# Kernel optimization log

Measured on AMD Instinct MI355X. Metric: run time of the kernel, lower is better.

Reference implementation:

```python
import jax, jax.numpy as jnp
import numpy as np

B, D, L = 16384, 1024, 3


def setup_inputs() -> dict:
    key = jax.random.key(0)
    kx, kw, kb = jax.random.split(key, 3)
    # xavier_normal for a (D, 1) tensor: std = sqrt(2 / (D + 1))
    std = float(np.sqrt(2.0 / (D + 1)))
    x = jax.random.normal(kx, (B, D), dtype=jnp.float32)
    weights = jax.random.normal(kw, (L, D), dtype=jnp.float32) * std
    bias = jax.random.normal(kb, (L, D), dtype=jnp.float32) * std
    return {"x": x, "weights": weights, "bias": bias}


def reference(x, weights, bias):
    # DCN cross layer: xl_{t+1} = x0 * (xl_t . w_t) + b_t + xl_t
    # (identical math to matmul(x0 xl^T, w) + b + xl, without the [B,D,D] intermediate)
    x0 = x

    def layer(xl, wb):
        w, b = wb  # [D], [D]
        s = xl @ w  # [B] scaled dot-product reduction
        xl_new = x0 * s[:, None] + b + xl  # [B, D]
        return xl_new, None

    out, _ = jax.lax.scan(layer, x, (weights, bias))
    return out
```

## Files before the change

kernel.cpp:

```cpp
#include <hip/hip_runtime.h>


#define CN_B 16384
#define CN_D 1024
#define CN_L 3
#define ROWS_PER_WAVE 2
#define WAVES_PER_BLOCK 4
#define ROWS_PER_BLOCK (ROWS_PER_WAVE * WAVES_PER_BLOCK)

__global__ __launch_bounds__(256, 4) void crossnet_kernel(
    const float* __restrict__ x,
    const float* __restrict__ w,
    const float* __restrict__ bias,
    float* __restrict__ out) {
  const int tid  = threadIdx.x;
  const int wave = tid >> 6;
  const int lane = tid & 63;
  const int row0 = (blockIdx.x * WAVES_PER_BLOCK + wave) * ROWS_PER_WAVE;

  const float4* xr0 = reinterpret_cast<const float4*>(x + (size_t)row0 * CN_D);
  const float4* xr1 = reinterpret_cast<const float4*>(x + (size_t)(row0 + 1) * CN_D);

  float4 x0a[4], xla[4], x0b[4], xlb[4];
  #pragma unroll
  for (int k = 0; k < 4; ++k) {
    x0a[k] = xr0[k * 64 + lane];
    x0b[k] = xr1[k * 64 + lane];
    xla[k] = x0a[k];
    xlb[k] = x0b[k];
  }

  #pragma unroll
  for (int l = 0; l < CN_L; ++l) {
    const float4* wrow = reinterpret_cast<const float4*>(w    + l * CN_D);
    const float4* brow = reinterpret_cast<const float4*>(bias + l * CN_D);
    float4 wl[4], bl[4];
    #pragma unroll
    for (int k = 0; k < 4; ++k) {
      wl[k] = wrow[k * 64 + lane];
      bl[k] = brow[k * 64 + lane];
    }

    float pa = 0.0f, pb = 0.0f;
    #pragma unroll
    for (int k = 0; k < 4; ++k) {
      pa += xla[k].x * wl[k].x; pb += xlb[k].x * wl[k].x;
      pa += xla[k].y * wl[k].y; pb += xlb[k].y * wl[k].y;
      pa += xla[k].z * wl[k].z; pb += xlb[k].z * wl[k].z;
      pa += xla[k].w * wl[k].w; pb += xlb[k].w * wl[k].w;
    }

    #pragma unroll
    for (int off = 32; off > 0; off >>= 1) {
      pa += __shfl_xor(pa, off, 64);
      pb += __shfl_xor(pb, off, 64);
    }

    #pragma unroll
    for (int k = 0; k < 4; ++k) {
      xla[k].x = x0a[k].x * pa + bl[k].x + xla[k].x;
      xla[k].y = x0a[k].y * pa + bl[k].y + xla[k].y;
      xla[k].z = x0a[k].z * pa + bl[k].z + xla[k].z;
      xla[k].w = x0a[k].w * pa + bl[k].w + xla[k].w;
      xlb[k].x = x0b[k].x * pb + bl[k].x + xlb[k].x;
      xlb[k].y = x0b[k].y * pb + bl[k].y + xlb[k].y;
      xlb[k].z = x0b[k].z * pb + bl[k].z + xlb[k].z;
      xlb[k].w = x0b[k].w * pb + bl[k].w + xlb[k].w;
    }
  }

  float4* or0 = reinterpret_cast<float4*>(out + (size_t)row0 * CN_D);
  float4* or1 = reinterpret_cast<float4*>(out + (size_t)(row0 + 1) * CN_D);
  #pragma unroll
  for (int k = 0; k < 4; ++k) {
    or0[k * 64 + lane] = xla[k];
    or1[k * 64 + lane] = xlb[k];
  }
}

extern "C" void kernel_launch(void* const* d_in, const int* in_sizes, int n_in,
                              void* d_out, int out_size, void* d_ws, size_t ws_size,
                              hipStream_t stream) {
  const float* x    = (const float*)d_in[0];
  const float* w    = (const float*)d_in[1];
  const float* bias = (const float*)d_in[2];
  float* out        = (float*)d_out;

  crossnet_kernel<<<CN_B / ROWS_PER_BLOCK, 256, 0, stream>>>(x, w, bias, out);
}
```

Before: 25.55 us.

## Collapse three cross layers into closed-form scalar recurrence with single batched reduction

Every layer's output has the form x0*alpha + accumulated bias, so the kernel precomputes all three x0·w_l dot products and the bias·weight constants in one pass. It then finishes every wave reduction in one batched shuffle phase instead of three serialized ones. The output is written as x0*alpha plus the summed bias. This removes the dependent reduction chain and the per-layer register updates. In exchange each lane carries more accumulators and loads all weights up front, and the floating-point summation order changes.

```diff
diff --git a/kernel.cpp b/kernel.cpp
--- a/kernel.cpp
+++ b/kernel.cpp
@@ -3,10 +3,13 @@
 
 #define CN_B 16384
 #define CN_D 1024
-#define CN_L 3
 #define ROWS_PER_WAVE 2
 #define WAVES_PER_BLOCK 4
 #define ROWS_PER_BLOCK (ROWS_PER_WAVE * WAVES_PER_BLOCK)
+
+__device__ __forceinline__ float dot4(const float4 a, const float4 b) {
+  return a.x * b.x + a.y * b.y + a.z * b.z + a.w * b.w;
+}
 
 __global__ __launch_bounds__(256, 4) void crossnet_kernel(
     const float* __restrict__ x,
@@ -20,61 +23,78 @@
 
   const float4* xr0 = reinterpret_cast<const float4*>(x + (size_t)row0 * CN_D);
   const float4* xr1 = reinterpret_cast<const float4*>(x + (size_t)(row0 + 1) * CN_D);
+  const float4* w0r = reinterpret_cast<const float4*>(w);
+  const float4* w1r = reinterpret_cast<const float4*>(w + CN_D);
+  const float4* w2r = reinterpret_cast<const float4*>(w + 2 * CN_D);
+  const float4* b0r = reinterpret_cast<const float4*>(bias);
+  const float4* b1r = reinterpret_cast<const float4*>(bias + CN_D);
+  const float4* b2r = reinterpret_cast<const float4*>(bias + 2 * CN_D);
 
-  float4 x0a[4], xla[4], x0b[4], xlb[4];
+  float4 x0a[4], x0b[4];
   #pragma unroll
   for (int k = 0; k < 4; ++k) {
     x0a[k] = xr0[k * 64 + lane];
     x0b[k] = xr1[k * 64 + lane];
-    xla[k] = x0a[k];
-    xlb[k] = x0b[k];
+  }
+
+  float da0 = 0.f, da1 = 0.f, da2 = 0.f;
+  float db0 = 0.f, db1 = 0.f, db2 = 0.f;
+  float c1 = 0.f, c2 = 0.f;
+  float4 bs[4];
+
+  #pragma unroll
+  for (int k = 0; k < 4; ++k) {
+    const int idx = k * 64 + lane;
+    const float4 w0 = w0r[idx];
+    const float4 w1 = w1r[idx];
+    const float4 w2 = w2r[idx];
+    const float4 b0 = b0r[idx];
+    const float4 b1 = b1r[idx];
+    const float4 b2 = b2r[idx];
+
+    da0 += dot4(x0a[k], w0);  db0 += dot4(x0b[k], w0);
+    da1 += dot4(x0a[k], w1);  db1 += dot4(x0b[k], w1);
+    da2 += dot4(x0a[k], w2);  db2 += dot4(x0b[k], w2);
+
+    c1 += dot4(b0, w1);
+    float4 b01;
+    b01.x = b0.x + b1.x; b01.y = b0.y + b1.y;
+    b01.z = b0.z + b1.z; b01.w = b0.w + b1.w;
+    c2 += dot4(b01, w2);
+    bs[k].x = b01.x + b2.x; bs[k].y = b01.y + b2.y;
+    bs[k].z = b01.z + b2.z; bs[k].w = b01.w + b2.w;
   }
 
   #pragma unroll
-  for (int l = 0; l < CN_L; ++l) {
-    const float4* wrow = reinterpret_cast<const float4*>(w    + l * CN_D);
-    const float4* brow = reinterpret_cast<const float4*>(bias + l * CN_D);
-    float4 wl[4], bl[4];
-    #pragma unroll
-    for (int k = 0; k < 4; ++k) {
-      wl[k] = wrow[k * 64 + lane];
-      bl[k] = brow[k * 64 + lane];
-    }
+  for (int off = 32; off > 0; off >>= 1) {
+    da0 += __shfl_xor(da0, off, 64);
+    da1 += __shfl_xor(da1, off, 64);
+    da2 += __shfl_xor(da2, off, 64);
+    db0 += __shfl_xor(db0, off, 64);
+    db1 += __shfl_xor(db1, off, 64);
+    db2 += __shfl_xor(db2, off, 64);
+    c1  += __shfl_xor(c1,  off, 64);
+    c2  += __shfl_xor(c2,  off, 64);
+  }
 
-    float pa = 0.0f, pb = 0.0f;
-    #pragma unroll
-    for (int k = 0; k < 4; ++k) {
-      pa += xla[k].x * wl[k].x; pb += xlb[k].x * wl[k].x;
-      pa += xla[k].y * wl[k].y; pb += xlb[k].y * wl[k].y;
-      pa += xla[k].z * wl[k].z; pb += xlb[k].z * wl[k].z;
-      pa += xla[k].w * wl[k].w; pb += xlb[k].w * wl[k].w;
-    }
-
-    #pragma unroll
-    for (int off = 32; off > 0; off >>= 1) {
-      pa += __shfl_xor(pa, off, 64);
-      pb += __shfl_xor(pb, off, 64);
-    }
-
-    #pragma unroll
-    for (int k = 0; k < 4; ++k) {
-      xla[k].x = x0a[k].x * pa + bl[k].x + xla[k].x;
-      xla[k].y = x0a[k].y * pa + bl[k].y + xla[k].y;
-      xla[k].z = x0a[k].z * pa + bl[k].z + xla[k].z;
-      xla[k].w = x0a[k].w * pa + bl[k].w + xla[k].w;
-      xlb[k].x = x0b[k].x * pb + bl[k].x + xlb[k].x;
-      xlb[k].y = x0b[k].y * pb + bl[k].y + xlb[k].y;
-      xlb[k].z = x0b[k].z * pb + bl[k].z + xlb[k].z;
-      xlb[k].w = x0b[k].w * pb + bl[k].w + xlb[k].w;
-    }
-  }
+  float aa = 1.0f + da0;
+  aa = aa + (aa * da1 + c1);
+  aa = aa + (aa * da2 + c2);
+  float ab = 1.0f + db0;
+  ab = ab + (ab * db1 + c1);
+  ab = ab + (ab * db2 + c2);
 
   float4* or0 = reinterpret_cast<float4*>(out + (size_t)row0 * CN_D);
   float4* or1 = reinterpret_cast<float4*>(out + (size_t)(row0 + 1) * CN_D);
   #pragma unroll
   for (int k = 0; k < 4; ++k) {
-    or0[k * 64 + lane] = xla[k];
-    or1[k * 64 + lane] = xlb[k];
+    float4 oa, ob;
+    oa.x = x0a[k].x * aa + bs[k].x;  ob.x = x0b[k].x * ab + bs[k].x;
+    oa.y = x0a[k].y * aa + bs[k].y;  ob.y = x0b[k].y * ab + bs[k].y;
+    oa.z = x0a[k].z * aa + bs[k].z;  ob.z = x0b[k].z * ab + bs[k].z;
+    oa.w = x0a[k].w * aa + bs[k].w;  ob.w = x0b[k].w * ab + bs[k].w;
+    or0[k * 64 + lane] = oa;
+    or1[k * 64 + lane] = ob;
   }
 }
 
```

Result: slower. 26.20 us (+2.6%).
